# Performance work log

Hardware: AMD Instinct MI355X
Metric: run time of the kernel (lower is better)

The kernel has to match this reference:

```python
import jax, jax.numpy as jnp
import numpy as np

NUM_ITERATIONS = 3


def squash(s, axis=-1):
    # v = (|s|^2 / (1+|s|^2)) * s / |s|  (standard CapsNet squash)
    sq_norm = jnp.sum(s * s, axis=axis, keepdims=True)
    return (sq_norm / (1.0 + sq_norm)) * s / jnp.sqrt(sq_norm + 1e-9)


def setup_inputs() -> dict:
    key = jax.random.key(0)
    k1, k2 = jax.random.split(key)
    B, IN_C, OUT_C, OUT_D, IN_D = 64, 2048, 32, 16, 8
    x = jax.random.normal(k1, (B, IN_C, IN_D), dtype=jnp.float32)
    W = jax.random.normal(k2, (1, IN_C, OUT_C, OUT_D, IN_D), dtype=jnp.float32)
    return {"x": x, "W": W}


def reference(x, W):
    # u_hat[b,i,o,d] = sum_m W[0,i,o,d,m] * x[b,i,m]
    u_hat = jnp.einsum('iodm,bim->biod', W[0], x)  # [B, IN_C, OUT_C, OUT_D]
    B, IN_C, OUT_C, _ = u_hat.shape
    b_logits = jnp.zeros((B, IN_C, OUT_C), dtype=u_hat.dtype)
    v = None
    for _ in range(NUM_ITERATIONS):
        # PyTorch F.softmax(b) with implicit dim=1 for a 4-D tensor -> softmax over in_channels
        c = jax.nn.softmax(b_logits, axis=1)               # [B, IN_C, OUT_C]
        s = jnp.einsum('bio,biod->bod', c, u_hat)          # [B, OUT_C, OUT_D]
        v = squash(s)                                      # [B, OUT_C, OUT_D]
        b_logits = b_logits + jnp.einsum('biod,bod->bio', u_hat, v)
    return v
```

## Files before the change

kernel.cpp:

```cpp
#include <hip/hip_runtime.h>
#include <math.h>

#define B_ 64
#define IC 2048
#define OC 32
#define OD 16
#define ID 8

typedef __attribute__((ext_vector_type(8)))  short s16x8;
typedef __attribute__((ext_vector_type(16))) float f32x16;

#define GLOAD_LDS16(gp, lp)                                                       \
  __builtin_amdgcn_global_load_lds((const __attribute__((address_space(1))) void*)(gp), \
                                   (__attribute__((address_space(3))) void*)(lp), \
                                   16, 0, 0)

__device__ __forceinline__ unsigned short f2bf(float f) {
  unsigned u = __float_as_uint(f);
  return (unsigned short)((u + 0x7fffu + ((u >> 16) & 1u)) >> 16);
}
__device__ __forceinline__ float bf2f(unsigned short h) {
  return __uint_as_float(((unsigned)h) << 16);
}
__device__ __forceinline__ f32x16 mfma16(s16x8 a, s16x8 b, f32x16 c) {
  return __builtin_amdgcn_mfma_f32_32x32x16_bf16(a, b, c, 0, 0, 0);
}
__device__ __forceinline__ float dot8(const float4 w0, const float4 w1,
                                      const float4 xa, const float4 xb) {
  return w0.x*xa.x + w0.y*xa.y + w0.z*xa.z + w0.w*xa.w
       + w1.x*xb.x + w1.y*xb.y + w1.z*xb.z + w1.w*xb.w;
}

__global__ __launch_bounds__(256) void convW(const float* __restrict__ W,
                                             unsigned short* __restrict__ Wbf) {
  const int e4 = blockIdx.x * 256 + threadIdx.x;
  const float4 v = ((const float4*)W)[e4];
  const int i = e4 >> 10;
  const int r = (e4 & 1023) << 2;
  ushort4 h, l;
  h.x = f2bf(v.x); l.x = f2bf(v.x - bf2f(h.x));
  h.y = f2bf(v.y); l.y = f2bf(v.y - bf2f(h.y));
  h.z = f2bf(v.z); l.z = f2bf(v.z - bf2f(h.z));
  h.w = f2bf(v.w); l.w = f2bf(v.w - bf2f(h.w));
  *(ushort4*)&Wbf[(size_t)i * 8192 + r]        = h;
  *(ushort4*)&Wbf[(size_t)i * 8192 + 4096 + r] = l;
}

__global__ __launch_bounds__(256) void convX(const float* __restrict__ x,
                                             unsigned short* __restrict__ xb) {
  const int idx = blockIdx.x * 256 + threadIdx.x;
  const int m2 = idx & 1, i = (idx >> 1) & 2047, b = idx >> 12;
  const float4 v = *(const float4*)(x + (size_t)b * 16384 + i * 8 + m2 * 4);
  ushort4 h, l;
  h.x = f2bf(v.x); l.x = f2bf(v.x - bf2f(h.x));
  h.y = f2bf(v.y); l.y = f2bf(v.y - bf2f(h.y));
  h.z = f2bf(v.z); l.z = f2bf(v.z - bf2f(h.z));
  h.w = f2bf(v.w); l.w = f2bf(v.w - bf2f(h.w));
  *(ushort4*)&xb[(size_t)i * 1024 + b * 8 + m2 * 4]       = h;
  *(ushort4*)&xb[(size_t)i * 1024 + 512 + b * 8 + m2 * 4] = l;
}

template<bool WEIGHTED, int NCH>
__global__ __launch_bounds__(256) void fusedM(
    const unsigned short* __restrict__ Wbf, const unsigned short* __restrict__ xb,
    const float* __restrict__ vss, float* __restrict__ part,
    float* __restrict__ zpart)
{
  constexpr int CI = IC / NCH;
  const int t     = threadIdx.x;
  const int ch    = blockIdx.x % NCH;
  const int q     = blockIdx.x / NCH;
  const int lane  = t & 63;
  const int wv    = t >> 6;
  const int s     = q * 4 + wv;
  const int opair = s >> 1;
  const int bt    = s & 1;
  const int l31   = lane & 31;
  const int hb    = lane >> 5;
  const int i0    = ch * CI;

  const unsigned short* ap =
      Wbf + (size_t)i0 * 8192 + opair * 256 + (l31 >> 4) * 128 + (lane & 15) * 8;
  const unsigned short* bp =
      xb + (size_t)i0 * 1024 + hb * 512 + bt * 256 + l31 * 8;

  f32x16 acc = (f32x16)0.0f;
  float zA = 0.f, zB = 0.f;
  float vsr[16];

  if constexpr (WEIGHTED) {
    const float* vp = vss + s * 1024 + hb * 32 + l31;
#pragma unroll
    for (int r = 0; r < 16; ++r) vsr[r] = vp[r * 64];
  }

  s16x8 AH[3], AL[3], BV[3];
  AH[0] = *(const s16x8*)ap;
  AL[0] = *(const s16x8*)(ap + 4096);
  BV[0] = *(const s16x8*)bp;
  if (CI > 1) {
    AH[1] = *(const s16x8*)(ap + 8192);
    AL[1] = *(const s16x8*)(ap + 8192 + 4096);
    BV[1] = *(const s16x8*)(bp + 1024);
  }

#pragma unroll
  for (int ii = 0; ii < CI; ++ii) {
    const int cs = ii % 3;
    const int ns = (ii + 2) % 3;
    if (ii + 2 < CI) {
      AH[ns] = *(const s16x8*)(ap + (size_t)(ii + 2) * 8192);
      AL[ns] = *(const s16x8*)(ap + (size_t)(ii + 2) * 8192 + 4096);
      BV[ns] = *(const s16x8*)(bp + (size_t)(ii + 2) * 1024);
    }

    if constexpr (!WEIGHTED) {
      acc = mfma16(AH[cs], BV[cs], acc);
      acc = mfma16(AL[cs], BV[cs], acc);
    } else {
      f32x16 u = mfma16(AH[cs], BV[cs], (f32x16)0.0f);
      u = mfma16(AL[cs], BV[cs], u);
      float pdA = 0.f, pdB = 0.f;
#pragma unroll
      for (int r = 0; r < 8; ++r)  pdA = fmaf(u[r], vsr[r], pdA);
#pragma unroll
      for (int r = 8; r < 16; ++r) pdB = fmaf(u[r], vsr[r], pdB);
      pdA += __shfl_xor(pdA, 32);
      pdB += __shfl_xor(pdB, 32);
      const float pA = __expf(pdA), pB = __expf(pdB);
#pragma unroll
      for (int r = 0; r < 8; ++r)  acc[r] = fmaf(pA, u[r], acc[r]);
#pragma unroll
      for (int r = 8; r < 16; ++r) acc[r] = fmaf(pB, u[r], acc[r]);
      zA += pA; zB += pB;
    }
  }

  float* op = part + (size_t)ch * 32768;
#pragma unroll
  for (int r = 0; r < 16; ++r)
    op[(s * 16 + r) * 64 + hb * 32 + l31] = acc[r];
  if constexpr (WEIGHTED) {
    if (lane < 32) {
      zpart[(size_t)ch * 2048 + (s * 2 + 0) * 32 + lane] = zA;
      zpart[(size_t)ch * 2048 + (s * 2 + 1) * 32 + lane] = zB;
    }
  }
}

template<int PASS, int NCH>
__global__ __launch_bounds__(512) void rsqM(
    const float* __restrict__ part, const float* __restrict__ zpart,
    float* __restrict__ vss, float* __restrict__ out)
{
  __shared__ float rzs[32];
  __shared__ float sqs[512];
  const int t   = threadIdx.x;
  const int blk = blockIdx.x;
  const int s   = blk >> 1, oo = blk & 1;
  const int l31 = t & 31, hb = (t >> 5) & 1, rr = t >> 6;
  const size_t tid = (size_t)blk * 512 + t;

  float acc = 0.f;
#pragma unroll 8
  for (int ch = 0; ch < NCH; ++ch) acc += part[(size_t)ch * 32768 + tid];

  if constexpr (PASS == 0) {
    if (t < 32) rzs[t] = 1.f / 2048.f;
  } else {
    if (t < 32) {
      float zs = 0.f;
#pragma unroll 8
      for (int ch = 0; ch < NCH; ++ch)
        zs += zpart[(size_t)ch * 2048 + (s * 2 + oo) * 32 + t];
      rzs[t] = 1.f / zs;
    }
  }
  __syncthreads();
  const float sv = acc * rzs[l31];
  sqs[t] = sv * sv;
  __syncthreads();
  float sq = 0.f;
#pragma unroll
  for (int k = 0; k < 16; ++k) sq += sqs[l31 + k * 32];
  const float f = (sq / (1.f + sq)) * rsqrtf(sq + 1e-9f);
  const float v = sv * f;

  if constexpr (PASS == 0)      vss[tid] = v;
  else if constexpr (PASS == 1) vss[tid] += v;
  else {
    const int b = (s & 1) * 32 + l31;
    const int o = (s >> 1) * 2 + oo;
    const int d = (rr & 3) + 8 * (rr >> 2) + 4 * hb;
    out[(b * 32 + o) * 16 + d] = v;
  }
}

template<bool WEIGHTED, int NCH>
__global__ __launch_bounds__(512) void fusedF32(
    const float* __restrict__ x, const float* __restrict__ W,
    const float* __restrict__ vs, float* __restrict__ part,
    float* __restrict__ zpart)
{
  constexpr int CI  = IC / NCH;
  constexpr int NSW = CI / 8;
  const int t    = threadIdx.x;
  const int xcd  = blockIdx.x & 7;
  const int q    = blockIdx.x >> 3;
  const int ch   = (q >> 2) * 8 + xcd;
  const int bh   = q & 3;
  const int lane = t & 63;
  const int wv   = t >> 6;
  const int og   = wv >> 2;
  const int bset = wv & 3;
  const int op   = lane >> 2;
  const int dq   = lane & 3;
  const int o    = og * 16 + op;
  const int rot  = lane & 7;
  const int i0   = ch * CI;
  const int jb   = o * 32 + dq * 8;
  const int bl0  = bset * 4;
  const int b0   = bh * 16 + bl0;

  __shared__ float Wbuf[2][4096];
  __shared__ float xall[1024];

  const float4* Wg = (const float4*)W;
  const float4* xg = (const float4*)x;

  float4 acc[4];
  float  zacc[4];
  float4 vreg[4];
#pragma unroll
  for (int k = 0; k < 4; ++k) { acc[k] = make_float4(0,0,0,0); zacc[k] = 0.f; }

  if constexpr (WEIGHTED) {
#pragma unroll
    for (int bb = 0; bb < 4; ++bb)
      vreg[bb] = *(const float4*)(vs + ((size_t)(b0 + bb) * 32 + o) * 16 + dq * 4);
  }

  auto stageW = [&](int i, int nb) {
    const float4* Wi = Wg + (size_t)i * 1024;
#pragma unroll
    for (int k = 0; k < 2; ++k) {
      const int p   = wv * 128 + k * 64 + lane;
      const int src = (p & ~7) | ((p & 7) ^ ((p >> 3) & 7));
      GLOAD_LDS16(Wi + src, &Wbuf[nb][(wv * 128 + k * 64) * 4]);
    }
  };
  auto stageX = [&](int sw) {
    if (t < 256) {
      const int b = t >> 4, r = t & 15;
      const int ia = i0 + sw * 8 + (r >> 1);
      GLOAD_LDS16(xg + ((size_t)(bh * 16 + b) * IC + ia) * 2 + (r & 1),
                  &xall[(wv * 64) * 4]);
    }
  };

  stageX(0);
  stageW(i0, 0);
  int cur = 0;

#pragma unroll 1
  for (int sw = 0; sw < NSW; ++sw) {
#pragma unroll 1
    for (int j = 0; j < 8; ++j) {
      const int ii = sw * 8 + j;
      __syncthreads();
      if (ii + 1 < CI) stageW(i0 + ii + 1, cur ^ 1);

      const float* Wb = &Wbuf[cur][0];
      float4 wr[8];
#pragma unroll
      for (int r = 0; r < 8; ++r)
        wr[r] = *(const float4*)&Wb[(jb + (r ^ rot)) * 4];

#pragma unroll
      for (int bb = 0; bb < 4; ++bb) {
        const int bl = bl0 + bb;
        const float4 xa = *(const float4*)&xall[bl * 64 + j * 8];
        const float4 xc = *(const float4*)&xall[bl * 64 + j * 8 + 4];
        float4 u;
        u.x = dot8(wr[0], wr[1], xa, xc);
        u.y = dot8(wr[2], wr[3], xa, xc);
        u.z = dot8(wr[4], wr[5], xa, xc);
        u.w = dot8(wr[6], wr[7], xa, xc);
        if constexpr (!WEIGHTED) {
          acc[bb].x += u.x; acc[bb].y += u.y; acc[bb].z += u.z; acc[bb].w += u.w;
        } else {
          const float4 vv = vreg[bb];
          float pd = u.x * vv.x + u.y * vv.y + u.z * vv.z + u.w * vv.w;
          pd += __shfl_xor(pd, 1);
          pd += __shfl_xor(pd, 2);
          const float p = __expf(pd);
          acc[bb].x = fmaf(p, u.x, acc[bb].x);
          acc[bb].y = fmaf(p, u.y, acc[bb].y);
          acc[bb].z = fmaf(p, u.z, acc[bb].z);
          acc[bb].w = fmaf(p, u.w, acc[bb].w);
          zacc[bb] += p;
        }
      }
      cur ^= 1;
    }
    if (sw + 1 < NSW) { __syncthreads(); stageX(sw + 1); }
  }

  float4* part4 = (float4*)part;
#pragma unroll
  for (int bb = 0; bb < 4; ++bb) {
    const int b = b0 + bb;
    part4[((size_t)ch * 64 + b) * 128 + o * 4 + dq] = acc[bb];
    if constexpr (WEIGHTED) {
      if (dq == 0) zpart[(size_t)ch * 2048 + b * 32 + o] = zacc[bb];
    }
  }
}

template<int PASS, int NCH>
__global__ __launch_bounds__(256) void reduceSquash(
    const float* __restrict__ part, const float* __restrict__ rz,
    float* __restrict__ vsio, float* __restrict__ out)
{
  const int g = blockIdx.x * 256 + threadIdx.x;
  float s = 0.f;
#pragma unroll 8
  for (int ch = 0; ch < NCH; ++ch) s += part[(size_t)ch * 32768 + g];
  if constexpr (PASS == 0) s *= (1.f / 2048.f);
  else                     s *= rz[g >> 4];

  float sq = s * s;
#pragma unroll
  for (int k = 1; k < 16; k <<= 1) sq += __shfl_xor(sq, k);
  const float f = (sq / (1.f + sq)) * rsqrtf(sq + 1e-9f);
  const float v = s * f;

  if constexpr (PASS == 0)      vsio[g] = v;
  else if constexpr (PASS == 1) vsio[g] += v;
  else                          out[g] = v;
}

template<int NCH>
__global__ __launch_bounds__(256) void zredK(
    const float* __restrict__ zpart, float* __restrict__ rz)
{
  const int j = blockIdx.x * 256 + threadIdx.x;
  float zs = 0.f;
#pragma unroll 8
  for (int ch = 0; ch < NCH; ++ch) zs += zpart[(size_t)ch * 2048 + j];
  rz[j] = 1.f / zs;
}

extern "C" void kernel_launch(void* const* d_in, const int* in_sizes, int n_in,
                              void* d_out, int out_size, void* d_ws, size_t ws_size,
                              hipStream_t stream) {
  (void)in_sizes; (void)n_in; (void)out_size;
  const float* x = (const float*)d_in[0];
  const float* W = (const float*)d_in[1];
  float* out = (float*)d_out;
  float* ws  = (float*)d_ws;

  const size_t WBF_US = (size_t)IC * 8192;
  const size_t XB_US  = (size_t)IC * 1024;

  auto runM = [&](auto tag) {
    constexpr int NCH = decltype(tag)::value;
    float* part  = ws;
    float* zpart = part + (size_t)NCH * 32768;
    float* vsb   = zpart + (size_t)NCH * 2048;
    unsigned short* Wbf = (unsigned short*)(vsb + 32768);
    unsigned short* xbp = Wbf + WBF_US;

    const dim3 b256(256), b512(512), gF(8 * NCH), gR(64);
    convW<<<dim3(8192), b256, 0, stream>>>(W, Wbf);
    convX<<<dim3(1024), b256, 0, stream>>>(x, xbp);
    fusedM<false, NCH><<<gF, b256, 0, stream>>>(Wbf, xbp, nullptr, part, nullptr);
    rsqM<0, NCH><<<gR, b512, 0, stream>>>(part, nullptr, vsb, nullptr);
    fusedM<true, NCH><<<gF, b256, 0, stream>>>(Wbf, xbp, vsb, part, zpart);
    rsqM<1, NCH><<<gR, b512, 0, stream>>>(part, zpart, vsb, nullptr);
    fusedM<true, NCH><<<gF, b256, 0, stream>>>(Wbf, xbp, vsb, part, zpart);
    rsqM<2, NCH><<<gR, b512, 0, stream>>>(part, zpart, nullptr, out);
  };

  auto runF = [&](auto tag) {
    constexpr int NCH = decltype(tag)::value;
    float* part  = ws;
    float* zpart = part + (size_t)NCH * 32768;
    float* rz    = zpart + (size_t)NCH * 2048;
    float* vsb   = rz + 2048;

    const dim3 gF(4 * NCH), bF(512), b256(256), gR(128);
    fusedF32<false, NCH><<<gF, bF, 0, stream>>>(x, W, nullptr, part, nullptr);
    reduceSquash<0, NCH><<<gR, b256, 0, stream>>>(part, nullptr, vsb, nullptr);
    fusedF32<true, NCH><<<gF, bF, 0, stream>>>(x, W, vsb, part, zpart);
    zredK<NCH><<<dim3(8), b256, 0, stream>>>(zpart, rz);
    reduceSquash<1, NCH><<<gR, b256, 0, stream>>>(part, rz, vsb, nullptr);
    fusedF32<true, NCH><<<gF, bF, 0, stream>>>(x, W, vsb, part, zpart);
    zredK<NCH><<<dim3(8), b256, 0, stream>>>(zpart, rz);
    reduceSquash<2, NCH><<<gR, b256, 0, stream>>>(part, rz, nullptr, out);
  };

  auto needM = [&](size_t nch) -> size_t {
    return (nch * 32768 + nch * 2048 + 32768) * 4 + (WBF_US + XB_US) * 2;
  };
  const size_t needF256 = ((size_t)256 * 32768 + 256ul * 2048 + 2048 + 32768) * 4;

  if      (ws_size >= needM(128)) runM(std::integral_constant<int, 128>{});
  else if (ws_size >= needM(64))  runM(std::integral_constant<int, 64>{});
  else if (ws_size >= needF256)   runF(std::integral_constant<int, 256>{});
  else                            runF(std::integral_constant<int, 64>{});
}
```

Before: 96.63 us.

## Fuse bf16 split conversion of W and x into first routing pass

Removes the separate convW and convX kernels and folds the hi/lo bf16 conversion into the first unweighted pass. That pass now reads fp32 W and x directly, converts them in registers, runs the MFMAs, and writes the converted operands for later passes from one subset of waves. This saves two launches and a full extra read of W. In exchange the first pass does conversion ALU work and redundant conversions across waves, and its fp32 x loads are strided.

Result: no change. 96.98 us (+0.4%).

```diff
diff --git a/kernel.cpp b/kernel.cpp
--- a/kernel.cpp
+++ b/kernel.cpp
@@ -25,46 +25,27 @@
 __device__ __forceinline__ f32x16 mfma16(s16x8 a, s16x8 b, f32x16 c) {
   return __builtin_amdgcn_mfma_f32_32x32x16_bf16(a, b, c, 0, 0, 0);
 }
+__device__ __forceinline__ void cvt8(const float4 a, const float4 b,
+                                     s16x8& hi, s16x8& lo) {
+  const float v[8] = {a.x, a.y, a.z, a.w, b.x, b.y, b.z, b.w};
+#pragma unroll
+  for (int j = 0; j < 8; ++j) {
+    const unsigned short h = f2bf(v[j]);
+    hi[j] = (short)h;
+    lo[j] = (short)f2bf(v[j] - bf2f(h));
+  }
+}
 __device__ __forceinline__ float dot8(const float4 w0, const float4 w1,
                                       const float4 xa, const float4 xb) {
   return w0.x*xa.x + w0.y*xa.y + w0.z*xa.z + w0.w*xa.w
        + w1.x*xb.x + w1.y*xb.y + w1.z*xb.z + w1.w*xb.w;
 }
 
-__global__ __launch_bounds__(256) void convW(const float* __restrict__ W,
-                                             unsigned short* __restrict__ Wbf) {
-  const int e4 = blockIdx.x * 256 + threadIdx.x;
-  const float4 v = ((const float4*)W)[e4];
-  const int i = e4 >> 10;
-  const int r = (e4 & 1023) << 2;
-  ushort4 h, l;
-  h.x = f2bf(v.x); l.x = f2bf(v.x - bf2f(h.x));
-  h.y = f2bf(v.y); l.y = f2bf(v.y - bf2f(h.y));
-  h.z = f2bf(v.z); l.z = f2bf(v.z - bf2f(h.z));
-  h.w = f2bf(v.w); l.w = f2bf(v.w - bf2f(h.w));
-  *(ushort4*)&Wbf[(size_t)i * 8192 + r]        = h;
-  *(ushort4*)&Wbf[(size_t)i * 8192 + 4096 + r] = l;
-}
-
-__global__ __launch_bounds__(256) void convX(const float* __restrict__ x,
-                                             unsigned short* __restrict__ xb) {
-  const int idx = blockIdx.x * 256 + threadIdx.x;
-  const int m2 = idx & 1, i = (idx >> 1) & 2047, b = idx >> 12;
-  const float4 v = *(const float4*)(x + (size_t)b * 16384 + i * 8 + m2 * 4);
-  ushort4 h, l;
-  h.x = f2bf(v.x); l.x = f2bf(v.x - bf2f(h.x));
-  h.y = f2bf(v.y); l.y = f2bf(v.y - bf2f(h.y));
-  h.z = f2bf(v.z); l.z = f2bf(v.z - bf2f(h.z));
-  h.w = f2bf(v.w); l.w = f2bf(v.w - bf2f(h.w));
-  *(ushort4*)&xb[(size_t)i * 1024 + b * 8 + m2 * 4]       = h;
-  *(ushort4*)&xb[(size_t)i * 1024 + 512 + b * 8 + m2 * 4] = l;
-}
-
-template<bool WEIGHTED, int NCH>
-__global__ __launch_bounds__(256) void fusedM(
-    const unsigned short* __restrict__ Wbf, const unsigned short* __restrict__ xb,
-    const float* __restrict__ vss, float* __restrict__ part,
-    float* __restrict__ zpart)
+template<int NCH>
+__global__ __launch_bounds__(256) void convFused(
+    const float* __restrict__ x, const float* __restrict__ W,
+    unsigned short* __restrict__ Wbf, unsigned short* __restrict__ xbp,
+    float* __restrict__ part)
 {
   constexpr int CI = IC / NCH;
   const int t     = threadIdx.x;
@@ -79,6 +60,78 @@
   const int hb    = lane >> 5;
   const int i0    = ch * CI;
 
+  const int aeo = opair * 256 + (l31 >> 4) * 128 + (lane & 15) * 8;
+  const float* wp = W + (size_t)i0 * 4096 + aeo;
+  const float* xp = x + ((size_t)(bt * 32 + l31) * IC + i0) * ID;
+
+  f32x16 acc = (f32x16)0.0f;
+
+  float4 WA[3][2], XA[3][2];
+#pragma unroll
+  for (int p = 0; p < 2; ++p) {
+    if (p < CI) {
+      WA[p][0] = *(const float4*)(wp + (size_t)p * 4096);
+      WA[p][1] = *(const float4*)(wp + (size_t)p * 4096 + 4);
+      XA[p][0] = *(const float4*)(xp + (size_t)p * ID);
+      XA[p][1] = *(const float4*)(xp + (size_t)p * ID + 4);
+    }
+  }
+
+#pragma unroll
+  for (int ii = 0; ii < CI; ++ii) {
+    const int cs = ii % 3;
+    const int ns = (ii + 2) % 3;
+    if (ii + 2 < CI) {
+      WA[ns][0] = *(const float4*)(wp + (size_t)(ii + 2) * 4096);
+      WA[ns][1] = *(const float4*)(wp + (size_t)(ii + 2) * 4096 + 4);
+      XA[ns][0] = *(const float4*)(xp + (size_t)(ii + 2) * ID);
+      XA[ns][1] = *(const float4*)(xp + (size_t)(ii + 2) * ID + 4);
+    }
+
+    s16x8 aH, aL, xh, xl;
+    cvt8(WA[cs][0], WA[cs][1], aH, aL);
+    cvt8(XA[cs][0], XA[cs][1], xh, xl);
+    const s16x8 bv = hb ? xl : xh;
+
+    acc = mfma16(aH, bv, acc);
+    acc = mfma16(aL, bv, acc);
+
+    const int i = i0 + ii;
+    if (bt == 0 && lane < 32) {
+      *(s16x8*)(Wbf + (size_t)i * 8192 + aeo)        = aH;
+      *(s16x8*)(Wbf + (size_t)i * 8192 + 4096 + aeo) = aL;
+    }
+    if (opair == 0 && lane < 32) {
+      *(s16x8*)(xbp + (size_t)i * 1024 + bt * 256 + l31 * 8)       = xh;
+      *(s16x8*)(xbp + (size_t)i * 1024 + 512 + bt * 256 + l31 * 8) = xl;
+    }
+  }
+
+  float* op = part + (size_t)ch * 32768;
+#pragma unroll
+  for (int r = 0; r < 16; ++r)
+    op[(s * 16 + r) * 64 + hb * 32 + l31] = acc[r];
+}
+
+template<int NCH>
+__global__ __launch_bounds__(256) void fusedM(
+    const unsigned short* __restrict__ Wbf, const unsigned short* __restrict__ xb,
+    const float* __restrict__ vss, float* __restrict__ part,
+    float* __restrict__ zpart)
+{
+  constexpr int CI = IC / NCH;
+  const int t     = threadIdx.x;
+  const int ch    = blockIdx.x % NCH;
+  const int q     = blockIdx.x / NCH;
+  const int lane  = t & 63;
+  const int wv    = t >> 6;
+  const int s     = q * 4 + wv;
+  const int opair = s >> 1;
+  const int bt    = s & 1;
+  const int l31   = lane & 31;
+  const int hb    = lane >> 5;
+  const int i0    = ch * CI;
+
   const unsigned short* ap =
       Wbf + (size_t)i0 * 8192 + opair * 256 + (l31 >> 4) * 128 + (lane & 15) * 8;
   const unsigned short* bp =
@@ -88,7 +141,7 @@
   float zA = 0.f, zB = 0.f;
   float vsr[16];
 
-  if constexpr (WEIGHTED) {
+  {
     const float* vp = vss + s * 1024 + hb * 32 + l31;
 #pragma unroll
     for (int r = 0; r < 16; ++r) vsr[r] = vp[r * 64];
@@ -114,37 +167,30 @@
       BV[ns] = *(const s16x8*)(bp + (size_t)(ii + 2) * 1024);
     }
 
-    if constexpr (!WEIGHTED) {
-      acc = mfma16(AH[cs], BV[cs], acc);
-      acc = mfma16(AL[cs], BV[cs], acc);
-    } else {
-      f32x16 u = mfma16(AH[cs], BV[cs], (f32x16)0.0f);
-      u = mfma16(AL[cs], BV[cs], u);
-      float pdA = 0.f, pdB = 0.f;
-#pragma unroll
-      for (int r = 0; r < 8; ++r)  pdA = fmaf(u[r], vsr[r], pdA);
-#pragma unroll
-      for (int r = 8; r < 16; ++r) pdB = fmaf(u[r], vsr[r], pdB);
-      pdA += __shfl_xor(pdA, 32);
-      pdB += __shfl_xor(pdB, 32);
-      const float pA = __expf(pdA), pB = __expf(pdB);
-#pragma unroll
-      for (int r = 0; r < 8; ++r)  acc[r] = fmaf(pA, u[r], acc[r]);
-#pragma unroll
-      for (int r = 8; r < 16; ++r) acc[r] = fmaf(pB, u[r], acc[r]);
-      zA += pA; zB += pB;
-    }
+    f32x16 u = mfma16(AH[cs], BV[cs], (f32x16)0.0f);
+    u = mfma16(AL[cs], BV[cs], u);
+    float pdA = 0.f, pdB = 0.f;
+#pragma unroll
+    for (int r = 0; r < 8; ++r)  pdA = fmaf(u[r], vsr[r], pdA);
+#pragma unroll
+    for (int r = 8; r < 16; ++r) pdB = fmaf(u[r], vsr[r], pdB);
+    pdA += __shfl_xor(pdA, 32);
+    pdB += __shfl_xor(pdB, 32);
+    const float pA = __expf(pdA), pB = __expf(pdB);
+#pragma unroll
+    for (int r = 0; r < 8; ++r)  acc[r] = fmaf(pA, u[r], acc[r]);
+#pragma unroll
+    for (int r = 8; r < 16; ++r) acc[r] = fmaf(pB, u[r], acc[r]);
+    zA += pA; zB += pB;
   }
 
   float* op = part + (size_t)ch * 32768;
 #pragma unroll
   for (int r = 0; r < 16; ++r)
     op[(s * 16 + r) * 64 + hb * 32 + l31] = acc[r];
-  if constexpr (WEIGHTED) {
-    if (lane < 32) {
-      zpart[(size_t)ch * 2048 + (s * 2 + 0) * 32 + lane] = zA;
-      zpart[(size_t)ch * 2048 + (s * 2 + 1) * 32 + lane] = zB;
-    }
+  if (lane < 32) {
+    zpart[(size_t)ch * 2048 + (s * 2 + 0) * 32 + lane] = zA;
+    zpart[(size_t)ch * 2048 + (s * 2 + 1) * 32 + lane] = zB;
   }
 }
 
@@ -372,13 +418,11 @@
     unsigned short* xbp = Wbf + WBF_US;
 
     const dim3 b256(256), b512(512), gF(8 * NCH), gR(64);
-    convW<<<dim3(8192), b256, 0, stream>>>(W, Wbf);
-    convX<<<dim3(1024), b256, 0, stream>>>(x, xbp);
-    fusedM<false, NCH><<<gF, b256, 0, stream>>>(Wbf, xbp, nullptr, part, nullptr);
+    convFused<NCH><<<gF, b256, 0, stream>>>(x, W, Wbf, xbp, part);
     rsqM<0, NCH><<<gR, b512, 0, stream>>>(part, nullptr, vsb, nullptr);
-    fusedM<true, NCH><<<gF, b256, 0, stream>>>(Wbf, xbp, vsb, part, zpart);
+    fusedM<NCH><<<gF, b256, 0, stream>>>(Wbf, xbp, vsb, part, zpart);
     rsqM<1, NCH><<<gR, b512, 0, stream>>>(part, zpart, vsb, nullptr);
-    fusedM<true, NCH><<<gF, b256, 0, stream>>>(Wbf, xbp, vsb, part, zpart);
+    fusedM<NCH><<<gF, b256, 0, stream>>>(Wbf, xbp, vsb, part, zpart);
     rsqM<2, NCH><<<gR, b512, 0, stream>>>(part, zpart, nullptr, out);
   };
 
```
